# Kernel optimization log

Hardware: AMD Instinct MI355X
Metric: run time of the kernel (lower is better)

The kernel has to match this reference:

```python
import jax, jax.numpy as jnp
import numpy as np

DIM = 256
D_STATE = 16
D_CONV = 4
EXPAND = 2
D_INNER = DIM * EXPAND          # 512
DT_RANK = DIM // 16             # 16


def _dwconv(x_bcl, w, b, pad):
    # depthwise 1d conv; x_bcl: (B, C, L), w: (C, 1, K)
    out = jax.lax.conv_general_dilated(
        x_bcl, w, window_strides=(1,), padding=[pad],
        feature_group_count=x_bcl.shape[1],
        dimension_numbers=('NCH', 'OIH', 'NCH'))
    return out + b[None, :, None]


def _forward(x, ln_w, ln_b, W_in, conv_w, conv_b, W_xproj, W_dt, b_dt,
             A_log, D_ssm, W_outp, c1_w, c1_b, c2_w, c2_b, c3_w, c3_b,
             W_out, b_out, W_skip, b_skip):
    Bsz, C = x.shape[:2]
    img_dims = x.shape[2:]
    L = int(np.prod(img_dims))
    xf = x.reshape(Bsz, C, L).transpose(0, 2, 1)          # (B, L, C)
    # LayerNorm over channel dim
    mu = jnp.mean(xf, axis=-1, keepdims=True)
    var = jnp.var(xf, axis=-1, keepdims=True)
    xn = (xf - mu) / jnp.sqrt(var + 1e-5) * ln_w + ln_b   # (B, L, C)

    # ---------------- Mamba block ----------------
    xz = xn @ W_in.T                                      # (B, L, 2*Di)
    xi, z = jnp.split(xz, 2, axis=-1)
    k = conv_w.shape[-1]
    # causal depthwise conv (pad left d_conv-1, truncate to L), then silu
    xc = _dwconv(xi.transpose(0, 2, 1), conv_w, conv_b, (k - 1, 0))
    xc = jax.nn.silu(xc).transpose(0, 2, 1)               # (B, L, Di)
    x_dbl = xc @ W_xproj.T                                # (B, L, dt_rank + 2*N)
    dt = x_dbl[..., :DT_RANK]
    B_s = x_dbl[..., DT_RANK:DT_RANK + D_STATE]           # (B, L, N)
    C_s = x_dbl[..., DT_RANK + D_STATE:]                  # (B, L, N)
    delta = jax.nn.softplus(dt @ W_dt.T + b_dt)           # (B, L, Di)
    A = -jnp.exp(A_log)                                   # (Di, N)
    dA = jnp.exp(delta[..., None] * A)                    # (B, L, Di, N)
    dBu = (delta * xc)[..., None] * B_s[:, :, None, :]    # (B, L, Di, N)

    def step(h, inp):
        dA_t, dBu_t, c_t = inp
        h = dA_t * h + dBu_t                              # (B, Di, N)
        y = jnp.einsum('bdn,bn->bd', h, c_t)
        return h, y

    h0 = jnp.zeros((Bsz, D_INNER, D_STATE), dtype=x.dtype)
    _, ys = jax.lax.scan(
        step, h0,
        (dA.transpose(1, 0, 2, 3), dBu.transpose(1, 0, 2, 3), C_s.transpose(1, 0, 2)))
    y = ys.transpose(1, 0, 2) + D_ssm * xc                # (B, L, Di)
    y = y * jax.nn.silu(z)
    x_ssm = y @ W_outp.T                                  # (B, L, C)

    # ---------------- multi-scale depthwise convs ----------------
    xnT = xn.transpose(0, 2, 1)                           # (B, C, L)

    def msconv(w, b):
        kk = w.shape[-1]
        return jax.nn.silu(_dwconv(xnT, w, b, (kk // 2, kk // 2))).transpose(0, 2, 1)

    combined = x_ssm + msconv(c1_w, c1_b) + msconv(c2_w, c2_b) + msconv(c3_w, c3_b)
    out = combined @ W_out.T + b_out + xn @ W_skip.T + b_skip
    out = out.transpose(0, 2, 1).reshape(x.shape)
    return out + x


def setup_inputs() -> dict:
    key = jax.random.key(0)
    ks = jax.random.split(key, 12)

    def rn(k, shape, s=0.02):
        return jax.random.normal(k, shape, dtype=jnp.float32) * s

    return {
        'x': jax.random.normal(ks[0], (2, DIM, 64, 64), dtype=jnp.float32),
        'ln_w': jnp.ones((DIM,), jnp.float32),
        'ln_b': jnp.zeros((DIM,), jnp.float32),
        'W_in': rn(ks[1], (2 * D_INNER, DIM)),
        'conv_w': rn(ks[2], (D_INNER, 1, D_CONV), 0.1),
        'conv_b': jnp.zeros((D_INNER,), jnp.float32),
        'W_xproj': rn(ks[3], (DT_RANK + 2 * D_STATE, D_INNER)),
        'W_dt': rn(ks[4], (D_INNER, DT_RANK), 0.1),
        'b_dt': jnp.full((D_INNER,), -4.0, jnp.float32),  # softplus(-4) ~ 0.018, stable dt
        'A_log': jnp.log(jnp.broadcast_to(
            jnp.arange(1, D_STATE + 1, dtype=jnp.float32), (D_INNER, D_STATE))),
        'D_ssm': jnp.ones((D_INNER,), jnp.float32),
        'W_outp': rn(ks[5], (DIM, D_INNER)),
        'c1_w': rn(ks[6], (DIM, 1, 3), 0.1),
        'c1_b': jnp.zeros((DIM,), jnp.float32),
        'c2_w': rn(ks[7], (DIM, 1, 5), 0.1),
        'c2_b': jnp.zeros((DIM,), jnp.float32),
        'c3_w': rn(ks[8], (DIM, 1, 7), 0.1),
        'c3_b': jnp.zeros((DIM,), jnp.float32),
        'W_out': rn(ks[9], (DIM, DIM)),
        'b_out': jnp.zeros((DIM,), jnp.float32),
        'W_skip': rn(ks[10], (DIM, DIM)),
        'b_skip': jnp.zeros((DIM,), jnp.float32),
    }


def reference(x, ln_w, ln_b, W_in, conv_w, conv_b, W_xproj, W_dt, b_dt,
              A_log, D_ssm, W_outp, c1_w, c1_b, c2_w, c2_b, c3_w, c3_b,
              W_out, b_out, W_skip, b_skip):
    return _forward(x, ln_w, ln_b, W_in, conv_w, conv_b, W_xproj, W_dt, b_dt,
                    A_log, D_ssm, W_outp, c1_w, c1_b, c2_w, c2_b, c3_w, c3_b,
                    W_out, b_out, W_skip, b_skip)
```

## Files before the change

kernel.cpp:

```cpp
#include <hip/hip_runtime.h>
#include <hip/hip_bf16.h>
#include <math.h>
#include <cstddef>

#define BSZ 2
#define DM 256
#define LSEQ 4096
#define DIN 512
#define DXZ 1024
#define DS 16
#define RANK 16
#define GXP 48
#define LC 32
#define NC 128
#define CSTRIDE (BSZ * DIN * 16)

typedef __attribute__((ext_vector_type(8))) short short8;
typedef __attribute__((ext_vector_type(4))) float f32x4;
struct bf4 { __hip_bfloat16 v[4]; };

__device__ __forceinline__ float silu_f(float x){ return x / (1.f + __expf(-x)); }
__device__ __forceinline__ float softplus_f(float x){ return fmaxf(x, 0.f) + log1pf(__expf(-fabsf(x))); }
__device__ __forceinline__ float b2f(__hip_bfloat16 v){ return __bfloat162float(v); }
__device__ __forceinline__ __hip_bfloat16 f2b(float v){ return __float2bfloat16(v); }

__device__ __forceinline__ void gl_lds16(const void* g, void* s){
    __builtin_amdgcn_global_load_lds((const __attribute__((address_space(1))) void*)g,
                                     (__attribute__((address_space(3))) void*)s, 16, 0, 0);
}

__global__ __launch_bounds__(256) void k_ln(const float* __restrict__ x,
                                            const float* __restrict__ lnw,
                                            const float* __restrict__ lnb,
                                            __hip_bfloat16* __restrict__ xnb){
    __shared__ float tile[DM * 33];
    __shared__ float rsum[8][32], rsq[8][32];
    __shared__ float mu_s[32], rs_s[32];
    int b  = blockIdx.x >> 7;
    int l0 = (blockIdx.x & 127) << 5;
    int tid = threadIdx.x;
    const float* xb = x + (size_t)b * DM * LSEQ;
    int lls = tid & 31, chi = tid >> 5;
    for (int cc = 0; cc < 32; ++cc){
        int c = cc * 8 + chi;
        tile[c * 33 + lls] = xb[(size_t)c * LSEQ + l0 + lls];
    }
    __syncthreads();
    int part = tid >> 5, l = tid & 31;
    float s = 0.f, sq = 0.f;
    for (int i = 0; i < 32; ++i){
        float v = tile[(part * 32 + i) * 33 + l];
        s += v; sq += v * v;
    }
    rsum[part][l] = s; rsq[part][l] = sq;
    __syncthreads();
    if (tid < 32){
        float ts = 0.f, tq = 0.f;
        for (int p = 0; p < 8; ++p){ ts += rsum[p][tid]; tq += rsq[p][tid]; }
        float mu  = ts * (1.f / DM);
        float var = tq * (1.f / DM) - mu * mu;
        mu_s[tid] = mu;
        rs_s[tid] = rsqrtf(var + 1e-5f);
    }
    __syncthreads();
    int c0 = tid & 63, lh = tid >> 6;
    for (int i = 0; i < 8; ++i){
        int ll = lh + 4 * i;
        float mu = mu_s[ll], rs = rs_s[ll];
        __hip_bfloat16* orow = xnb + (size_t)(b * LSEQ + l0 + ll) * 512;
        for (int j = 0; j < 4; ++j){
            int c = c0 + 64 * j;
            orow[c] = f2b((tile[c * 33 + ll] - mu) * rs * lnw[c] + lnb[c]);
        }
    }
}

__global__ __launch_bounds__(256) void k_cvtw(const float* __restrict__ W_in, const float* __restrict__ W_xproj,
                                              const float* __restrict__ W_outp, const float* __restrict__ W_out,
                                              const float* __restrict__ W_skip, const float* __restrict__ b_out,
                                              const float* __restrict__ b_skip,
                                              __hip_bfloat16* __restrict__ Winb, __hip_bfloat16* __restrict__ Wxpb,
                                              __hip_bfloat16* __restrict__ Wopb, __hip_bfloat16* __restrict__ Wcb,
                                              float* __restrict__ bc){
    int i0 = blockIdx.x * 256 + threadIdx.x;
    const int T = 256 * 256;
    for (int j = i0; j < 1024 * 256; j += T) Winb[j] = f2b(W_in[j]);
    for (int j = i0; j < 64 * 512; j += T){
        int r = j >> 9;
        Wxpb[j] = f2b(r < GXP ? W_xproj[r * 512 + (j & 511)] : 0.f);
    }
    for (int j = i0; j < 256 * 512; j += T) Wopb[j] = f2b(W_outp[j]);
    for (int j = i0; j < 256 * 512; j += T){
        int n = j >> 9, k = j & 511;
        Wcb[j] = f2b(k < 256 ? W_out[n * 256 + k] : W_skip[n * 256 + (k - 256)]);
    }
    if (i0 < 256) bc[i0] = b_out[i0] + b_skip[i0];
}

template<int EPI, int BM = 128>
__global__ __launch_bounds__(256) void k_mgemm(const __hip_bfloat16* __restrict__ A, int lda,
                                               const __hip_bfloat16* __restrict__ W,
                                               const float* __restrict__ bias,
                                               void* __restrict__ Cv, int ldc,
                                               int N, int K){
    constexpr int SA = BM / 8;
    constexpr int SAW = SA / 4;
    constexpr int WROWS = BM / 2;
    constexpr int MI = WROWS / 16;
    __shared__ __align__(16) __hip_bfloat16 As[BM * 64];
    __shared__ __align__(16) __hip_bfloat16 Ws[64 * 64];
    const int tid = threadIdx.x;
    const int wave = tid >> 6, lane = tid & 63;
    const int brow = blockIdx.x * BM, bcol = blockIdx.y * 64;
    const int wm = wave >> 1, wn = wave & 1;

    const int a_row = lane >> 3;
    const int a_chk = lane & 7;
    const int a_scol = ((a_chk ^ a_row) * 8);

    const int lrow = lane & 15;
    const int kc = lane >> 4;
    const int r7 = lrow & 7;

    f32x4 acc[MI][2] = {};

    for (int k0 = 0; k0 < K; k0 += 64){
#pragma unroll
        for (int j = 0; j < SAW; ++j){
            int seg = wave * SAW + j;
            const __hip_bfloat16* src = A + (size_t)(brow + seg * 8 + a_row) * lda + k0 + a_scol;
            gl_lds16(src, &As[seg * 512]);
        }
#pragma unroll
        for (int j = 0; j < 2; ++j){
            int seg = wave * 2 + j;
            const __hip_bfloat16* src = W + (size_t)(bcol + seg * 8 + a_row) * K + k0 + a_scol;
            gl_lds16(src, &Ws[seg * 512]);
        }
        __syncthreads();
#pragma unroll
        for (int kk = 0; kk < 2; ++kk){
            int kchunk = kk * 4 + kc;
            short8 af[MI], bfr[2];
#pragma unroll
            for (int mi = 0; mi < MI; ++mi){
                int row = wm * WROWS + mi * 16 + lrow;
                af[mi] = *(const short8*)&As[row * 64 + ((kchunk ^ r7) * 8)];
            }
#pragma unroll
            for (int ni = 0; ni < 2; ++ni){
                int row = wn * 32 + ni * 16 + lrow;
                bfr[ni] = *(const short8*)&Ws[row * 64 + ((kchunk ^ r7) * 8)];
            }
#pragma unroll
            for (int mi = 0; mi < MI; ++mi)
#pragma unroll
                for (int ni = 0; ni < 2; ++ni)
                    acc[mi][ni] = __builtin_amdgcn_mfma_f32_16x16x32_bf16(af[mi], bfr[ni], acc[mi][ni], 0, 0, 0);
        }
        __syncthreads();
    }

#pragma unroll
    for (int ni = 0; ni < 2; ++ni){
        int n = bcol + wn * 32 + ni * 16 + lrow;
        if (n >= N) continue;
        float bv = (EPI & 1) ? bias[n] : 0.f;
#pragma unroll
        for (int mi = 0; mi < MI; ++mi){
            int m0 = brow + wm * WROWS + mi * 16 + kc * 4;
#pragma unroll
            for (int r = 0; r < 4; ++r){
                float v = acc[mi][ni][r] + bv;
                if (EPI & 8) ((__hip_bfloat16*)Cv)[(size_t)(m0 + r) * ldc + n] = f2b(v);
                else         ((float*)Cv)[(size_t)(m0 + r) * ldc + n] = v;
            }
        }
    }
}

__global__ __launch_bounds__(256) void k_dtgemm(const float* __restrict__ A, int lda,
                                                const float* __restrict__ Wt,
                                                const float* __restrict__ bias,
                                                __hip_bfloat16* __restrict__ C, int ldc){
    __shared__ float As[16][68];
    __shared__ float Ws[16][68];
    int bm = blockIdx.x * 64, bn = blockIdx.y * 64;
    int tid = threadIdx.x;
    int a_m = tid >> 2, a_k = (tid & 3) * 4;
    int tx = tid & 15, ty = tid >> 4;
    float acc[4][4] = {};
    {
        float4 av = *(const float4*)(A + (size_t)(bm + a_m) * lda + a_k);
        As[a_k + 0][a_m] = av.x; As[a_k + 1][a_m] = av.y;
        As[a_k + 2][a_m] = av.z; As[a_k + 3][a_m] = av.w;
        float4 wv = *(const float4*)(Wt + (size_t)(bn + a_m) * 16 + a_k);
        Ws[a_k + 0][a_m] = wv.x; Ws[a_k + 1][a_m] = wv.y;
        Ws[a_k + 2][a_m] = wv.z; Ws[a_k + 3][a_m] = wv.w;
        __syncthreads();
#pragma unroll
        for (int k = 0; k < 16; ++k){
            float4 a4 = *(const float4*)&As[k][ty * 4];
            float4 b4 = *(const float4*)&Ws[k][tx * 4];
            acc[0][0] += a4.x * b4.x; acc[0][1] += a4.x * b4.y; acc[0][2] += a4.x * b4.z; acc[0][3] += a4.x * b4.w;
            acc[1][0] += a4.y * b4.x; acc[1][1] += a4.y * b4.y; acc[1][2] += a4.y * b4.z; acc[1][3] += a4.y * b4.w;
            acc[2][0] += a4.z * b4.x; acc[2][1] += a4.z * b4.y; acc[2][2] += a4.z * b4.z; acc[2][3] += a4.z * b4.w;
            acc[3][0] += a4.w * b4.x; acc[3][1] += a4.w * b4.y; acc[3][2] += a4.w * b4.z; acc[3][3] += a4.w * b4.w;
        }
    }
    int n = bn + tx * 4;
    float4 bb = *(const float4*)(bias + n);
#pragma unroll
    for (int i = 0; i < 4; ++i){
        int m = bm + ty * 4 + i;
        __hip_bfloat16* cp = C + (size_t)m * ldc + n;
        cp[0] = f2b(softplus_f(acc[i][0] + bb.x));
        cp[1] = f2b(softplus_f(acc[i][1] + bb.y));
        cp[2] = f2b(softplus_f(acc[i][2] + bb.z));
        cp[3] = f2b(softplus_f(acc[i][3] + bb.w));
    }
}

__global__ __launch_bounds__(256) void k_conv(const __hip_bfloat16* __restrict__ xz,
                                              const float* __restrict__ cw,
                                              const float* __restrict__ cb,
                                              __hip_bfloat16* __restrict__ xc){
    int idx = blockIdx.x * 256 + threadIdx.x;
    int d4 = (idx & 127) * 4;
    int bl = idx >> 7;
    int l  = bl & (LSEQ - 1);
    const __hip_bfloat16* base = xz + (size_t)bl * DXZ + d4;
    float4 bias = *(const float4*)(cb + d4);
    float acc[4] = {bias.x, bias.y, bias.z, bias.w};
    float4 w0 = *(const float4*)(cw + (d4 + 0) * 4);
    float4 w1 = *(const float4*)(cw + (d4 + 1) * 4);
    float4 w2 = *(const float4*)(cw + (d4 + 2) * 4);
    float4 w3 = *(const float4*)(cw + (d4 + 3) * 4);
    const float* wj[4] = {(const float*)&w0, (const float*)&w1, (const float*)&w2, (const float*)&w3};
#pragma unroll
    for (int t = 0; t < 4; ++t){
        int ls = l - (3 - t);
        if (ls >= 0){
            bf4 v = *(const bf4*)(base - (size_t)(3 - t) * DXZ);
#pragma unroll
            for (int j = 0; j < 4; ++j) acc[j] += wj[j][t] * b2f(v.v[j]);
        }
    }
    bf4 o;
#pragma unroll
    for (int j = 0; j < 4; ++j) o.v[j] = f2b(silu_f(acc[j]));
    *(bf4*)(xc + (size_t)bl * DIN + d4) = o;
}

__global__ __launch_bounds__(512) void k_scan1(const __hip_bfloat16* __restrict__ delta,
                                               const __hip_bfloat16* __restrict__ xc,
                                               const float* __restrict__ xdbl,
                                               const float* __restrict__ A_log,
                                               float* __restrict__ Acar,
                                               float* __restrict__ Bcar){
    int bx = blockIdx.x;
    int dh = bx & 1;
    int c  = (bx >> 1) & (NC - 1);
    int b  = bx >> 8;
    int tid = threadIdx.x;
    int dloc = tid >> 1, nh = tid & 1;
    int d = dh * 256 + dloc;
    int n0 = nh * 8;
    __shared__ float Bs[LC][DS];
    {
        int t = tid >> 4, n = tid & 15;
        Bs[t][n] = xdbl[(size_t)(b * LSEQ + c * LC + t) * GXP + RANK + n];
    }
    __syncthreads();
    float Av[8];
    float a1 = -__expf(A_log[d * 16]);
    bool fast = true;
#pragma unroll
    for (int j = 0; j < 8; ++j){
        Av[j] = -__expf(A_log[d * 16 + n0 + j]);
        fast = fast && (fabsf(Av[j] - (float)(n0 + j + 1) * a1) <= 1e-4f * fabsf(Av[j]) + 1e-7f);
    }
    float ap[8], ac[8];
#pragma unroll
    for (int j = 0; j < 8; ++j){ ap[j] = 1.f; ac[j] = 0.f; }
    const __hip_bfloat16* dp = delta + (size_t)(b * LSEQ + c * LC) * DIN + d;
    const __hip_bfloat16* xp = xc    + (size_t)(b * LSEQ + c * LC) * DIN + d;
    if (fast){
        for (int t = 0; t < LC; ++t){
            float de = b2f(dp[(size_t)t * DIN]);
            float u  = de * b2f(xp[(size_t)t * DIN]);
            float p  = __expf(de * a1);
            float p2 = p * p, p4 = p2 * p2, p8 = p4 * p4;
            float da = nh ? p8 * p : p;
#pragma unroll
            for (int j = 0; j < 8; ++j){
                ap[j] *= da;
                ac[j] = da * ac[j] + u * Bs[t][n0 + j];
                da *= p;
            }
        }
    } else {
        for (int t = 0; t < LC; ++t){
            float de = b2f(dp[(size_t)t * DIN]);
            float u  = de * b2f(xp[(size_t)t * DIN]);
#pragma unroll
            for (int j = 0; j < 8; ++j){
                float da = __expf(de * Av[j]);
                ap[j] *= da;
                ac[j] = da * ac[j] + u * Bs[t][n0 + j];
            }
        }
    }
    size_t o = (size_t)c * CSTRIDE + (size_t)(b * DIN + d) * 16 + n0;
    *(float4*)(Acar + o)     = make_float4(ap[0], ap[1], ap[2], ap[3]);
    *(float4*)(Acar + o + 4) = make_float4(ap[4], ap[5], ap[6], ap[7]);
    *(float4*)(Bcar + o)     = make_float4(ac[0], ac[1], ac[2], ac[3]);
    *(float4*)(Bcar + o + 4) = make_float4(ac[4], ac[5], ac[6], ac[7]);
}

__global__ __launch_bounds__(256) void k_scan2(const float* __restrict__ Acar,
                                               const float* __restrict__ Bcar,
                                               float* __restrict__ hinit){
    __shared__ float a_s[NC][33];
    __shared__ float b_s[NC][33];
    __shared__ float h_s[NC][33];
    const int tid = threadIdx.x;
    const int idx0 = blockIdx.x * 32;
    const int s_ld = tid & 31, cr = tid >> 5;
#pragma unroll
    for (int r = 0; r < 16; ++r){
        int c = r * 8 + cr;
        size_t g = (size_t)c * CSTRIDE + idx0 + s_ld;
        a_s[c][s_ld] = Acar[g];
        b_s[c][s_ld] = Bcar[g];
    }
    __syncthreads();
    const int lane = tid & 63, w = tid >> 6;
#pragma unroll
    for (int i = 0; i < 8; ++i){
        int s = w * 8 + i;
        float a0 = a_s[2 * lane][s],     b0 = b_s[2 * lane][s];
        float a1 = a_s[2 * lane + 1][s], b1 = b_s[2 * lane + 1][s];
        float av = a0 * a1, bv = a1 * b0 + b1;
#pragma unroll
        for (int d2 = 1; d2 < 64; d2 <<= 1){
            float ao = __shfl_up(av, d2);
            float bo = __shfl_up(bv, d2);
            if (lane >= d2){ bv = av * bo + bv; av = ao * av; }
        }
        float ax = __shfl_up(av, 1), bx = __shfl_up(bv, 1);
        if (lane == 0){ ax = 1.f; bx = 0.f; }
        h_s[2 * lane][s]     = bx;
        h_s[2 * lane + 1][s] = a0 * bx + b0;
    }
    __syncthreads();
#pragma unroll
    for (int r = 0; r < 16; ++r){
        int c = r * 8 + cr;
        hinit[(size_t)c * CSTRIDE + idx0 + s_ld] = h_s[c][s_ld];
    }
}

__global__ __launch_bounds__(512) void k_scan3(const __hip_bfloat16* __restrict__ delta,
                                               const __hip_bfloat16* __restrict__ xc,
                                               const __hip_bfloat16* __restrict__ xz,
                                               const float* __restrict__ xdbl,
                                               const float* __restrict__ A_log,
                                               const float* __restrict__ D_ssm,
                                               const float* __restrict__ hinit,
                                               __hip_bfloat16* __restrict__ y){
    int bx = blockIdx.x;
    int dh = bx & 1;
    int c  = (bx >> 1) & (NC - 1);
    int b  = bx >> 8;
    int tid = threadIdx.x;
    int dloc = tid >> 1, nh = tid & 1;
    int d = dh * 256 + dloc;
    int n0 = nh * 8;
    __shared__ float Bs[LC][DS], Cs[LC][DS];
    {
        int t = tid >> 4, n = tid & 15;
        size_t r = (size_t)(b * LSEQ + c * LC + t) * GXP;
        Bs[t][n] = xdbl[r + RANK + n];
        Cs[t][n] = xdbl[r + RANK + DS + n];
    }
    __syncthreads();
    float Av[8];
    float a1 = -__expf(A_log[d * 16]);
    bool fast = true;
#pragma unroll
    for (int j = 0; j < 8; ++j){
        Av[j] = -__expf(A_log[d * 16 + n0 + j]);
        fast = fast && (fabsf(Av[j] - (float)(n0 + j + 1) * a1) <= 1e-4f * fabsf(Av[j]) + 1e-7f);
    }
    float h[8];
    size_t ho = (size_t)c * CSTRIDE + (size_t)(b * DIN + d) * 16 + n0;
    {
        float4 h0 = *(const float4*)(hinit + ho);
        float4 h1 = *(const float4*)(hinit + ho + 4);
        h[0] = h0.x; h[1] = h0.y; h[2] = h0.z; h[3] = h0.w;
        h[4] = h1.x; h[5] = h1.y; h[6] = h1.z; h[7] = h1.w;
    }
    float Dd = D_ssm[d];
    size_t rb = (size_t)(b * LSEQ + c * LC);
    if (fast){
        for (int t = 0; t < LC; ++t){
            size_t row = rb + t;
            float de  = b2f(delta[row * DIN + d]);
            float xcv = b2f(xc[row * DIN + d]);
            float u = de * xcv;
            float p  = __expf(de * a1);
            float p2 = p * p, p4 = p2 * p2, p8 = p4 * p4;
            float da = nh ? p8 * p : p;
            float yv = 0.f;
#pragma unroll
            for (int j = 0; j < 8; ++j){
                h[j] = da * h[j] + u * Bs[t][n0 + j];
                yv += h[j] * Cs[t][n0 + j];
                da *= p;
            }
            yv += __shfl_xor(yv, 1);
            if (nh == 0){
                float zv = b2f(xz[row * DXZ + DIN + d]);
                y[row * DIN + d] = f2b((yv + Dd * xcv) * silu_f(zv));
            }
        }
    } else {
        for (int t = 0; t < LC; ++t){
            size_t row = rb + t;
            float de  = b2f(delta[row * DIN + d]);
            float xcv = b2f(xc[row * DIN + d]);
            float u = de * xcv;
            float yv = 0.f;
#pragma unroll
            for (int j = 0; j < 8; ++j){
                float da = __expf(de * Av[j]);
                h[j] = da * h[j] + u * Bs[t][n0 + j];
                yv += h[j] * Cs[t][n0 + j];
            }
            yv += __shfl_xor(yv, 1);
            if (nh == 0){
                float zv = b2f(xz[row * DXZ + DIN + d]);
                y[row * DIN + d] = f2b((yv + Dd * xcv) * silu_f(zv));
            }
        }
    }
}

__global__ __launch_bounds__(256) void k_msconv(const __hip_bfloat16* __restrict__ xnb,
                                                const __hip_bfloat16* __restrict__ xssm,
                                                const float* __restrict__ c1w, const float* __restrict__ c1b,
                                                const float* __restrict__ c2w, const float* __restrict__ c2b,
                                                const float* __restrict__ c3w, const float* __restrict__ c3b,
                                                __hip_bfloat16* __restrict__ Acomb){
    int idx = blockIdx.x * 256 + threadIdx.x;
    int cch = idx & (DM - 1);
    int bl  = idx >> 8;
    int l   = bl & (LSEQ - 1);
    int bL  = bl - l;
    float a1 = c1b[cch], a2 = c2b[cch], a3 = c3b[cch];
#pragma unroll
    for (int j = -3; j <= 3; ++j){
        int ll = l + j;
        if ((unsigned)ll < LSEQ){
            float v = b2f(xnb[(size_t)(bL + ll) * 512 + cch]);
            if (j >= -1 && j <= 1) a1 += c1w[cch * 3 + (j + 1)] * v;
            if (j >= -2 && j <= 2) a2 += c2w[cch * 5 + (j + 2)] * v;
            a3 += c3w[cch * 7 + (j + 3)] * v;
        }
    }
    float res = b2f(xssm[(size_t)bl * 256 + cch]) + silu_f(a1) + silu_f(a2) + silu_f(a3);
    Acomb[(size_t)bl * 512 + cch] = f2b(res);
}

__global__ __launch_bounds__(256) void k_out(const float* __restrict__ outlc,
                                             const float* __restrict__ x,
                                             float* __restrict__ out){
    __shared__ float tile[32][33];
    int bid = blockIdx.x;
    int lt = bid & 127;
    int ct = (bid >> 7) & 7;
    int b  = bid >> 10;
    int l0 = lt * 32, c0 = ct * 32;
    int tx = threadIdx.x & 31, ty = threadIdx.x >> 5;
    for (int r = 0; r < 32; r += 8)
        tile[ty + r][tx] = outlc[(size_t)(b * LSEQ + l0 + ty + r) * DM + c0 + tx];
    __syncthreads();
    for (int r = 0; r < 32; r += 8){
        int cc = c0 + ty + r;
        size_t o = (size_t)(b * DM + cc) * LSEQ + l0 + tx;
        out[o] = tile[tx][ty + r] + x[o];
    }
}

extern "C" void kernel_launch(void* const* d_in, const int* in_sizes, int n_in,
                              void* d_out, int out_size, void* d_ws, size_t ws_size,
                              hipStream_t stream){
    const float* x      = (const float*)d_in[0];
    const float* ln_w   = (const float*)d_in[1];
    const float* ln_b   = (const float*)d_in[2];
    const float* W_in   = (const float*)d_in[3];
    const float* conv_w = (const float*)d_in[4];
    const float* conv_b = (const float*)d_in[5];
    const float* W_xproj= (const float*)d_in[6];
    const float* W_dt   = (const float*)d_in[7];
    const float* b_dt   = (const float*)d_in[8];
    const float* A_log  = (const float*)d_in[9];
    const float* D_ssm  = (const float*)d_in[10];
    const float* W_outp = (const float*)d_in[11];
    const float* c1_w   = (const float*)d_in[12];
    const float* c1_b   = (const float*)d_in[13];
    const float* c2_w   = (const float*)d_in[14];
    const float* c2_b   = (const float*)d_in[15];
    const float* c3_w   = (const float*)d_in[16];
    const float* c3_b   = (const float*)d_in[17];
    const float* W_out  = (const float*)d_in[18];
    const float* b_out  = (const float*)d_in[19];
    const float* W_skip = (const float*)d_in[20];
    const float* b_skip = (const float*)d_in[21];
    float* out = (float*)d_out;

    char* base = (char*)d_ws;
    const size_t MB = 1024 * 1024;
    __hip_bfloat16* Acomb = (__hip_bfloat16*)(base);
    __hip_bfloat16* xzb   = (__hip_bfloat16*)(base + 8*MB);
    __hip_bfloat16* xcb   = (__hip_bfloat16*)(base + 24*MB);
    float*          xdbl  = (float*)        (base + 32*MB);
    __hip_bfloat16* deltab= (__hip_bfloat16*)(base + 34*MB);
    float*          Acar  = (float*)        (base + 42*MB);
    float*          Bcar  = (float*)        (base + 50*MB);
    float*          hinit = (float*)        (base + 58*MB);
    __hip_bfloat16* xssmb = (__hip_bfloat16*)(base + 66*MB);
    __hip_bfloat16* Winb  = (__hip_bfloat16*)(base + 70*MB);
    __hip_bfloat16* Wxpb  = (__hip_bfloat16*)(base + 70*MB + 512*1024);
    __hip_bfloat16* Wopb  = (__hip_bfloat16*)(base + 71*MB);
    __hip_bfloat16* Wcb   = (__hip_bfloat16*)(base + 71*MB + 256*1024);
    float*          bc    = (float*)        (base + 71*MB + 512*1024);
    __hip_bfloat16* xnb   = Acomb + 256;
    __hip_bfloat16* ybf   = (__hip_bfloat16*)Bcar;
    float*          outlc = Acar;

    const int M = BSZ * LSEQ;

    k_cvtw<<<dim3(256), dim3(256), 0, stream>>>(W_in, W_xproj, W_outp, W_out, W_skip, b_out, b_skip,
                                                Winb, Wxpb, Wopb, Wcb, bc);
    k_ln<<<dim3(256), dim3(256), 0, stream>>>(x, ln_w, ln_b, xnb);
    k_mgemm<8><<<dim3(64, 16), dim3(256), 0, stream>>>(xnb, 512, Winb, nullptr, xzb, DXZ, 1024, 256);
    k_conv<<<dim3(M * DIN / 4 / 256), dim3(256), 0, stream>>>(xzb, conv_w, conv_b, xcb);
    k_mgemm<0, 32><<<dim3(256, 1), dim3(256), 0, stream>>>(xcb, 512, Wxpb, nullptr, xdbl, GXP, GXP, 512);
    k_dtgemm<<<dim3(128, 8), dim3(256), 0, stream>>>(xdbl, GXP, W_dt, b_dt, deltab, DIN);
    k_scan1<<<dim3(BSZ * NC * 2), dim3(512), 0, stream>>>(deltab, xcb, xdbl, A_log, Acar, Bcar);
    k_scan2<<<dim3(512), dim3(256), 0, stream>>>(Acar, Bcar, hinit);
    k_scan3<<<dim3(BSZ * NC * 2), dim3(512), 0, stream>>>(deltab, xcb, xzb, xdbl, A_log, D_ssm, hinit, ybf);
    k_mgemm<8><<<dim3(64, 4), dim3(256), 0, stream>>>(ybf, 512, Wopb, nullptr, xssmb, 256, 256, 512);
    k_msconv<<<dim3(M * DM / 256), dim3(256), 0, stream>>>(xnb, xssmb, c1_w, c1_b, c2_w, c2_b, c3_w, c3_b, Acomb);
    k_mgemm<1><<<dim3(64, 4), dim3(256), 0, stream>>>(Acomb, 512, Wcb, bc, outlc, DM, 256, 512);
    k_out<<<dim3(2048), dim3(256), 0, stream>>>(outlc, x, out);
}
```

Baseline: 250.2 us.

## Fuse transpose and residual add into final GEMM epilogue; retune GEMM tile shapes

The final combined GEMM now writes its tile through shared memory, transposed, and adds the bias and the input residual directly into the output. This removes the separate k_out transpose kernel and the float intermediate round trip through memory. The GEMM template also gains a BN parameter: the in-projection GEMM uses 128x128 tiles, and the out-projection and final GEMMs use 64x64 tiles to launch more blocks. The trade-offs are extra shared memory for the transpose tile, and larger tiles raising register pressure for the in-projection GEMM.

```diff
diff --git a/kernel.cpp b/kernel.cpp
--- a/kernel.cpp
+++ b/kernel.cpp
@@ -97,21 +97,27 @@
     if (i0 < 256) bc[i0] = b_out[i0] + b_skip[i0];
 }
 
-template<int EPI, int BM = 128>
+template<int EPI, int BM = 128, int BN = 64>
 __global__ __launch_bounds__(256) void k_mgemm(const __hip_bfloat16* __restrict__ A, int lda,
                                                const __hip_bfloat16* __restrict__ W,
                                                const float* __restrict__ bias,
                                                void* __restrict__ Cv, int ldc,
-                                               int N, int K){
-    constexpr int SA = BM / 8;
+                                               int N, int K,
+                                               const float* __restrict__ xres = nullptr){
+    constexpr int SA  = BM / 8;
     constexpr int SAW = SA / 4;
+    constexpr int SB  = BN / 8;
+    constexpr int SBW = SB / 4;
     constexpr int WROWS = BM / 2;
+    constexpr int WCOLS = BN / 2;
     constexpr int MI = WROWS / 16;
+    constexpr int NI = WCOLS / 16;
     __shared__ __align__(16) __hip_bfloat16 As[BM * 64];
-    __shared__ __align__(16) __hip_bfloat16 Ws[64 * 64];
+    __shared__ __align__(16) __hip_bfloat16 Ws[BN * 64];
+    __shared__ float tileT[(EPI & 16) ? 64 * 65 : 1];
     const int tid = threadIdx.x;
     const int wave = tid >> 6, lane = tid & 63;
-    const int brow = blockIdx.x * BM, bcol = blockIdx.y * 64;
+    const int brow = blockIdx.x * BM, bcol = blockIdx.y * BN;
     const int wm = wave >> 1, wn = wave & 1;
 
     const int a_row = lane >> 3;
@@ -122,7 +128,7 @@
     const int kc = lane >> 4;
     const int r7 = lrow & 7;
 
-    f32x4 acc[MI][2] = {};
+    f32x4 acc[MI][NI] = {};
 
     for (int k0 = 0; k0 < K; k0 += 64){
 #pragma unroll
@@ -132,8 +138,8 @@
             gl_lds16(src, &As[seg * 512]);
         }
 #pragma unroll
-        for (int j = 0; j < 2; ++j){
-            int seg = wave * 2 + j;
+        for (int j = 0; j < SBW; ++j){
+            int seg = wave * SBW + j;
             const __hip_bfloat16* src = W + (size_t)(bcol + seg * 8 + a_row) * K + k0 + a_scol;
             gl_lds16(src, &Ws[seg * 512]);
         }
@@ -141,29 +147,54 @@
 #pragma unroll
         for (int kk = 0; kk < 2; ++kk){
             int kchunk = kk * 4 + kc;
-            short8 af[MI], bfr[2];
+            short8 af[MI], bfr[NI];
 #pragma unroll
             for (int mi = 0; mi < MI; ++mi){
                 int row = wm * WROWS + mi * 16 + lrow;
                 af[mi] = *(const short8*)&As[row * 64 + ((kchunk ^ r7) * 8)];
             }
 #pragma unroll
-            for (int ni = 0; ni < 2; ++ni){
-                int row = wn * 32 + ni * 16 + lrow;
+            for (int ni = 0; ni < NI; ++ni){
+                int row = wn * WCOLS + ni * 16 + lrow;
                 bfr[ni] = *(const short8*)&Ws[row * 64 + ((kchunk ^ r7) * 8)];
             }
 #pragma unroll
             for (int mi = 0; mi < MI; ++mi)
 #pragma unroll
-                for (int ni = 0; ni < 2; ++ni)
+                for (int ni = 0; ni < NI; ++ni)
                     acc[mi][ni] = __builtin_amdgcn_mfma_f32_16x16x32_bf16(af[mi], bfr[ni], acc[mi][ni], 0, 0, 0);
         }
         __syncthreads();
     }
 
-#pragma unroll
-    for (int ni = 0; ni < 2; ++ni){
-        int n = bcol + wn * 32 + ni * 16 + lrow;
+    if (EPI & 16){
+#pragma unroll
+        for (int ni = 0; ni < NI; ++ni){
+            int nl = wn * WCOLS + ni * 16 + lrow;
+#pragma unroll
+            for (int mi = 0; mi < MI; ++mi){
+                int ml = wm * WROWS + mi * 16 + kc * 4;
+#pragma unroll
+                for (int r = 0; r < 4; ++r)
+                    tileT[nl * 65 + ml + r] = acc[mi][ni][r];
+            }
+        }
+        __syncthreads();
+        int b = brow >> 12, l0 = brow & 4095;
+        int lr = tid & 63, nr = tid >> 6;
+        float* out = (float*)Cv;
+#pragma unroll
+        for (int rr = 0; rr < 16; ++rr){
+            int n = rr * 4 + nr;
+            size_t o = (size_t)(b * DM + bcol + n) * LSEQ + l0 + lr;
+            out[o] = tileT[n * 65 + lr] + bias[bcol + n] + xres[o];
+        }
+        return;
+    }
+
+#pragma unroll
+    for (int ni = 0; ni < NI; ++ni){
+        int n = bcol + wn * WCOLS + ni * 16 + lrow;
         if (n >= N) continue;
         float bv = (EPI & 1) ? bias[n] : 0.f;
 #pragma unroll
@@ -471,26 +502,6 @@
     }
     float res = b2f(xssm[(size_t)bl * 256 + cch]) + silu_f(a1) + silu_f(a2) + silu_f(a3);
     Acomb[(size_t)bl * 512 + cch] = f2b(res);
-}
-
-__global__ __launch_bounds__(256) void k_out(const float* __restrict__ outlc,
-                                             const float* __restrict__ x,
-                                             float* __restrict__ out){
-    __shared__ float tile[32][33];
-    int bid = blockIdx.x;
-    int lt = bid & 127;
-    int ct = (bid >> 7) & 7;
-    int b  = bid >> 10;
-    int l0 = lt * 32, c0 = ct * 32;
-    int tx = threadIdx.x & 31, ty = threadIdx.x >> 5;
-    for (int r = 0; r < 32; r += 8)
-        tile[ty + r][tx] = outlc[(size_t)(b * LSEQ + l0 + ty + r) * DM + c0 + tx];
-    __syncthreads();
-    for (int r = 0; r < 32; r += 8){
-        int cc = c0 + ty + r;
-        size_t o = (size_t)(b * DM + cc) * LSEQ + l0 + tx;
-        out[o] = tile[tx][ty + r] + x[o];
-    }
 }
 
 extern "C" void kernel_launch(void* const* d_in, const int* in_sizes, int n_in,
@@ -538,22 +549,20 @@
     float*          bc    = (float*)        (base + 71*MB + 512*1024);
     __hip_bfloat16* xnb   = Acomb + 256;
     __hip_bfloat16* ybf   = (__hip_bfloat16*)Bcar;
-    float*          outlc = Acar;
 
     const int M = BSZ * LSEQ;
 
     k_cvtw<<<dim3(256), dim3(256), 0, stream>>>(W_in, W_xproj, W_outp, W_out, W_skip, b_out, b_skip,
                                                 Winb, Wxpb, Wopb, Wcb, bc);
     k_ln<<<dim3(256), dim3(256), 0, stream>>>(x, ln_w, ln_b, xnb);
-    k_mgemm<8><<<dim3(64, 16), dim3(256), 0, stream>>>(xnb, 512, Winb, nullptr, xzb, DXZ, 1024, 256);
+    k_mgemm<8, 128, 128><<<dim3(64, 8), dim3(256), 0, stream>>>(xnb, 512, Winb, nullptr, xzb, DXZ, 1024, 256);
     k_conv<<<dim3(M * DIN / 4 / 256), dim3(256), 0, stream>>>(xzb, conv_w, conv_b, xcb);
-    k_mgemm<0, 32><<<dim3(256, 1), dim3(256), 0, stream>>>(xcb, 512, Wxpb, nullptr, xdbl, GXP, GXP, 512);
+    k_mgemm<0, 32, 64><<<dim3(256, 1), dim3(256), 0, stream>>>(xcb, 512, Wxpb, nullptr, xdbl, GXP, GXP, 512);
     k_dtgemm<<<dim3(128, 8), dim3(256), 0, stream>>>(xdbl, GXP, W_dt, b_dt, deltab, DIN);
     k_scan1<<<dim3(BSZ * NC * 2), dim3(512), 0, stream>>>(deltab, xcb, xdbl, A_log, Acar, Bcar);
     k_scan2<<<dim3(512), dim3(256), 0, stream>>>(Acar, Bcar, hinit);
     k_scan3<<<dim3(BSZ * NC * 2), dim3(512), 0, stream>>>(deltab, xcb, xzb, xdbl, A_log, D_ssm, hinit, ybf);
-    k_mgemm<8><<<dim3(64, 4), dim3(256), 0, stream>>>(ybf, 512, Wopb, nullptr, xssmb, 256, 256, 512);
+    k_mgemm<8, 64, 64><<<dim3(128, 4), dim3(256), 0, stream>>>(ybf, 512, Wopb, nullptr, xssmb, 256, 256, 512);
     k_msconv<<<dim3(M * DM / 256), dim3(256), 0, stream>>>(xnb, xssmb, c1_w, c1_b, c2_w, c2_b, c3_w, c3_b, Acomb);
-    k_mgemm<1><<<dim3(64, 4), dim3(256), 0, stream>>>(Acomb, 512, Wcb, bc, outlc, DM, 256, 512);
-    k_out<<<dim3(2048), dim3(256), 0, stream>>>(outlc, x, out);
-}
+    k_mgemm<17, 64, 64><<<dim3(128, 4), dim3(256), 0, stream>>>(Acomb, 512, Wcb, bc, out, DM, 256, 512, x);
+}
```

New measurement: 244.7 us. -2.2%, faster.
